# Kernel optimization log

Hardware: AMD Instinct MI355X
Metric: run time of the kernel (lower is better)

## Reference

```python
import jax, jax.numpy as jnp
import numpy as np

LMAX = 2
MMAX = 2
SPH = (LMAX + 1) ** 2  # 9 coefficients
E = 800000


def _rot_y(a):
    c, s = jnp.cos(a), jnp.sin(a)
    o, z = jnp.ones_like(a), jnp.zeros_like(a)
    return jnp.stack([jnp.stack([c, z, s], -1),
                      jnp.stack([z, o, z], -1),
                      jnp.stack([-s, z, c], -1)], -2)


def _rot_x(a):
    c, s = jnp.cos(a), jnp.sin(a)
    o, z = jnp.ones_like(a), jnp.zeros_like(a)
    return jnp.stack([jnp.stack([o, z, z], -1),
                      jnp.stack([z, c, -s], -1),
                      jnp.stack([z, s, c], -1)], -2)


def _z_rot_mat(angle, l):
    # e3nn _z_rot_mat: M[i, dim-1-i] = sin(f_i*angle); M[i, i] = cos(f_i*angle)
    dim = 2 * l + 1
    freqs = jnp.arange(l, -l - 1, -1, dtype=angle.dtype)  # (dim,)
    s = jnp.sin(freqs * angle[:, None])  # [E, dim]
    c = jnp.cos(freqs * angle[:, None])
    inds = jnp.arange(dim)
    M = jnp.zeros((angle.shape[0], dim, dim), angle.dtype)
    M = M.at[:, inds, dim - 1 - inds].set(s)
    M = M.at[:, inds, inds].set(c)  # center overwrites sin(0)=0, as in torch
    return M


def _wigner_D(l, alpha, beta, gamma, J):
    Xa = _z_rot_mat(alpha, l)
    Xb = _z_rot_mat(beta, l)
    Xc = _z_rot_mat(gamma, l)
    return Xa @ J @ Xb @ J @ Xc


def _build_to_m():
    # CoefficientMapping.to_m: permutation regrouping (l,m) coefficients by m
    idx = lambda l, m: l * l + l + m
    order = []
    for m in range(MMAX + 1):
        for l in range(m, LMAX + 1):
            order.append(idx(l, m))
        if m > 0:
            for l in range(m, LMAX + 1):
                order.append(idx(l, -m))
    to_m = np.zeros((SPH, SPH), np.float32)
    for row, col in enumerate(order):
        to_m[row, col] = 1.0
    return jnp.asarray(to_m)


def setup_inputs() -> dict:
    key = jax.random.key(0)
    k1, k2, k3, k4 = jax.random.split(key, 4)
    return {
        'edge_distance_vec': jax.random.normal(k1, (E, 3), jnp.float32),
        'rand_vec': jax.random.uniform(k2, (E, 3), jnp.float32),
        'Jd_1': jax.random.normal(k3, (3, 3), jnp.float32),
        'Jd_2': jax.random.normal(k4, (5, 5), jnp.float32),
        'to_m': _build_to_m(),
    }


def reference(edge_distance_vec, rand_vec, Jd_1, Jd_2, to_m):
    v = edge_distance_vec
    dtype = v.dtype
    # ---- init_edge_rot_mat (rot_clip=False since direct_forces=True) ----
    norm_x = v / jnp.linalg.norm(v, axis=1, keepdims=True)
    e2 = rand_vec - 0.5
    e2 = e2 / jnp.linalg.norm(e2, axis=1, keepdims=True)
    e2b = jnp.stack([-e2[:, 1], e2[:, 0], e2[:, 2]], axis=1)
    e2c = jnp.stack([e2[:, 0], -e2[:, 2], e2[:, 1]], axis=1)
    dot = lambda a: jnp.abs(jnp.sum(a * norm_x, axis=1, keepdims=True))
    e2 = jnp.where(dot(e2) > dot(e2b), e2b, e2)
    e2 = jnp.where(dot(e2) > dot(e2c), e2c, e2)
    norm_z = jnp.cross(norm_x, e2)
    norm_z = norm_z / jnp.linalg.norm(norm_z, axis=1, keepdims=True)
    norm_y = jnp.cross(norm_x, norm_z)
    norm_y = norm_y / jnp.linalg.norm(norm_y, axis=1, keepdims=True)
    R = jnp.stack([norm_z, norm_x, norm_y], axis=1)  # [E,3,3] rows z,x,y

    # ---- rotation_to_wigner: Euler angles (e3nn convention) ----
    x = R[:, :, 1]  # R @ e_y
    alpha = jnp.arctan2(x[:, 0], x[:, 2])
    beta = jnp.arccos(jnp.clip(x[:, 1], -1.0, 1.0))
    Ralign = _rot_y(alpha) @ _rot_x(beta) @ _rot_y(jnp.zeros_like(alpha))
    Rg = jnp.swapaxes(Ralign, 1, 2) @ R
    gamma = jnp.arctan2(Rg[:, 0, 2], Rg[:, 0, 0])

    Jd_0 = jnp.ones((1, 1), dtype)
    wigner = jnp.zeros((v.shape[0], SPH, SPH), dtype)
    start = 0
    for l, J in enumerate([Jd_0, Jd_1, Jd_2]):
        block = _wigner_D(l, alpha, beta, gamma, J.astype(dtype))
        wigner = wigner.at[:, start:start + 2 * l + 1,
                           start:start + 2 * l + 1].set(block)
        start += 2 * l + 1
    wigner_inv = jnp.swapaxes(wigner, 1, 2)  # lmax == mmax: no index_select

    wm = jnp.einsum('mk,nkj->nmj', to_m, wigner)
    wm_inv = jnp.einsum('njk,mk->njm', wigner_inv, to_m)
    return R, wm, wm_inv
```

## Files before the change

### kernel.cpp

```cpp
#include <hip/hip_runtime.h>
#include <hip/hip_bf16.h>
#include <math.h>

#define TPB 64

typedef float f32x4 __attribute__((ext_vector_type(4)));

__device__ __forceinline__ void wave_lds_fence() {
    __builtin_amdgcn_sched_barrier(0);
    asm volatile("s_waitcnt lgkmcnt(0)" ::: "memory");
    __builtin_amdgcn_sched_barrier(0);
}

template<int DIM>
__device__ __forceinline__ void zchain(
    const float* __restrict__ J,
    const float (&ca)[DIM], const float (&sa)[DIM],
    const float (&cb)[DIM], const float (&sb)[DIM],
    const float (&cc)[DIM], const float (&sc)[DIM],
    float (&D)[DIM][DIM])
{
    constexpr int d1 = DIM - 1;
    float Jl[DIM][DIM];
#pragma unroll
    for (int i = 0; i < DIM; ++i)
#pragma unroll
        for (int j = 0; j < DIM; ++j)
            Jl[i][j] = J[i * DIM + j];

    float U[DIM][DIM];
#pragma unroll
    for (int i = 0; i < DIM; ++i)
#pragma unroll
        for (int j = 0; j < DIM; ++j)
            U[i][j] = ca[i] * Jl[i][j] + sa[i] * Jl[d1 - i][j];

    float V[DIM][DIM];
#pragma unroll
    for (int i = 0; i < DIM; ++i)
#pragma unroll
        for (int j = 0; j < DIM; ++j)
            V[i][j] = U[i][j] * cb[j] + U[i][d1 - j] * sb[d1 - j];

    float W[DIM][DIM];
#pragma unroll
    for (int i = 0; i < DIM; ++i)
#pragma unroll
        for (int j = 0; j < DIM; ++j) {
            float acc = 0.f;
#pragma unroll
            for (int k = 0; k < DIM; ++k)
                acc = fmaf(V[i][k], Jl[k][j], acc);
            W[i][j] = acc;
        }
#pragma unroll
    for (int i = 0; i < DIM; ++i)
#pragma unroll
        for (int j = 0; j < DIM; ++j)
            D[i][j] = W[i][j] * cc[j] + W[i][d1 - j] * sc[d1 - j];
}


__global__ __launch_bounds__(TPB) void wigner_kernel(
    const float* __restrict__ vec, const float* __restrict__ rnd,
    const float* __restrict__ J1,  const float* __restrict__ J2,
    float* __restrict__ outR,
    float* __restrict__ outWm,
    float* __restrict__ outWi,
    int E)
{
    __shared__ __align__(16) float ldsR[TPB * 9];
    __shared__ __align__(16) float ldsW[TPB * 81];

    const int t  = threadIdx.x;
    const int e0 = blockIdx.x * TPB;
    const int e  = e0 + t;
    const int ei = (e < E) ? e : (E - 1);
    const int nvalid = min(TPB, E - e0);

    float vx = vec[3 * ei + 0], vy = vec[3 * ei + 1], vz = vec[3 * ei + 2];
    float rn = rsqrtf(vx * vx + vy * vy + vz * vz);
    float nx0 = vx * rn, nx1 = vy * rn, nx2 = vz * rn;

    float ox = rnd[3 * ei + 0] - 0.5f;
    float oy = rnd[3 * ei + 1] - 0.5f;
    float oz = rnd[3 * ei + 2] - 0.5f;
    float ro = rsqrtf(ox * ox + oy * oy + oz * oz);
    ox *= ro; oy *= ro; oz *= ro;

    float sx = ox, sy = oy, sz = oz;
    float dcur = fabsf(sx * nx0 + sy * nx1 + sz * nx2);
    {
        float bx = -oy, by = ox, bz = oz;
        float db = fabsf(bx * nx0 + by * nx1 + bz * nx2);
        if (dcur > db) { sx = bx; sy = by; sz = bz; dcur = db; }
        float cx = ox, cy = -oz, cz = oy;
        float dc = fabsf(cx * nx0 + cy * nx1 + cz * nx2);
        if (dcur > dc) { sx = cx; sy = cy; sz = cz; }
    }

    float zx = nx1 * sz - nx2 * sy;
    float zy = nx2 * sx - nx0 * sz;
    float zz = nx0 * sy - nx1 * sx;
    float rz = rsqrtf(zx * zx + zy * zy + zz * zz);
    zx *= rz; zy *= rz; zz *= rz;

    float yx = nx1 * zz - nx2 * zy;
    float yy = nx2 * zx - nx0 * zz;
    float yz = nx0 * zy - nx1 * zx;
    float ry = rsqrtf(yx * yx + yy * yy + yz * yz);
    yx *= ry; yy *= ry; yz *= ry;

    float h2a = zy * zy + yy * yy;
    float rha = rsqrtf(fmaxf(h2a, 1e-30f));
    bool  za  = (h2a < 1e-24f);
    float sa  = za ? 0.f : zy * rha;
    float caa = za ? 1.f : yy * rha;
    float cbb = fminf(1.f, fmaxf(-1.f, nx1));
    float sb  = sqrtf(fmaxf(0.f, 1.f - cbb * cbb));
    float gy  = caa * zz - sa * yz;
    float gx  = caa * zx - sa * yx;
    float h2g = gy * gy + gx * gx;
    float rhg = rsqrtf(fmaxf(h2g, 1e-30f));
    bool  zg  = (h2g < 1e-24f);
    float sg  = zg ? 0.f : gy * rhg;
    float cgg = zg ? 1.f : gx * rhg;

    float ca3[3] = {caa, 1.f, caa}, sa3[3] = {sa, 0.f, -sa};
    float cb3[3] = {cbb, 1.f, cbb}, sb3[3] = {sb, 0.f, -sb};
    float cc3[3] = {cgg, 1.f, cgg}, sc3[3] = {sg, 0.f, -sg};
    float D1[3][3];
    zchain<3>(J1, ca3, sa3, cb3, sb3, cc3, sc3, D1);

    float ca2 = caa * caa - sa * sa,  sa2 = 2.f * sa * caa;
    float cb2 = cbb * cbb - sb * sb,  sb2 = 2.f * sb * cbb;
    float cg2 = cgg * cgg - sg * sg,  sg2 = 2.f * sg * cgg;
    float ca5[5] = {ca2, caa, 1.f, caa, ca2}, sa5[5] = {sa2, sa, 0.f, -sa, -sa2};
    float cb5[5] = {cb2, cbb, 1.f, cbb, cb2}, sb5[5] = {sb2, sb, 0.f, -sb, -sb2};
    float cc5[5] = {cg2, cgg, 1.f, cgg, cg2}, sc5[5] = {sg2, sg, 0.f, -sg, -sg2};
    float D2[5][5];
    zchain<5>(J2, ca5, sa5, cb5, sb5, cc5, sc5, D2);

    {
        float* r9 = &ldsR[t * 9];
        r9[0] = zx;  r9[1] = zy;  r9[2] = zz;
        r9[3] = nx0; r9[4] = nx1; r9[5] = nx2;
        r9[6] = yx;  r9[7] = yy;  r9[8] = yz;

        float* w = &ldsW[t * 81];
        w[0] = 1.f;
#pragma unroll
        for (int c = 1; c < 9; ++c) w[c] = 0.f;
        w[9]  = 0.f; w[10] = D1[1][0]; w[11] = D1[1][1]; w[12] = D1[1][2];
#pragma unroll
        for (int c = 4; c < 9; ++c) w[9 + c] = 0.f;
#pragma unroll
        for (int c = 0; c < 4; ++c) w[18 + c] = 0.f;
#pragma unroll
        for (int c = 0; c < 5; ++c) w[22 + c] = D2[2][c];
        w[27] = 0.f; w[28] = D1[2][0]; w[29] = D1[2][1]; w[30] = D1[2][2];
#pragma unroll
        for (int c = 4; c < 9; ++c) w[27 + c] = 0.f;
#pragma unroll
        for (int c = 0; c < 4; ++c) w[36 + c] = 0.f;
#pragma unroll
        for (int c = 0; c < 5; ++c) w[40 + c] = D2[3][c];
        w[45] = 0.f; w[46] = D1[0][0]; w[47] = D1[0][1]; w[48] = D1[0][2];
#pragma unroll
        for (int c = 4; c < 9; ++c) w[45 + c] = 0.f;
#pragma unroll
        for (int c = 0; c < 4; ++c) w[54 + c] = 0.f;
#pragma unroll
        for (int c = 0; c < 5; ++c) w[58 + c] = D2[1][c];
#pragma unroll
        for (int c = 0; c < 4; ++c) w[63 + c] = 0.f;
#pragma unroll
        for (int c = 0; c < 5; ++c) w[67 + c] = D2[4][c];
#pragma unroll
        for (int c = 0; c < 4; ++c) w[72 + c] = 0.f;
#pragma unroll
        for (int c = 0; c < 5; ++c) w[76 + c] = D2[0][c];
    }
    wave_lds_fence();

    if (nvalid == TPB) {
        const f32x4* sR = reinterpret_cast<const f32x4*>(ldsR);
        f32x4* dR = reinterpret_cast<f32x4*>(outR + (size_t)e0 * 9);
#pragma unroll
        for (int idx = t; idx < (TPB * 9) / 4; idx += TPB)
            __builtin_nontemporal_store(sR[idx], &dR[idx]);
        const f32x4* sW = reinterpret_cast<const f32x4*>(ldsW);
        f32x4* dW = reinterpret_cast<f32x4*>(outWm + (size_t)e0 * 81);
        for (int idx = t; idx < (TPB * 81) / 4; idx += TPB)
            __builtin_nontemporal_store(sW[idx], &dW[idx]);
    } else {
        float* dR = outR + (size_t)e0 * 9;
        for (int idx = t; idx < nvalid * 9; idx += TPB) dR[idx] = ldsR[idx];
        float* dW = outWm + (size_t)e0 * 81;
        for (int idx = t; idx < nvalid * 81; idx += TPB) dW[idx] = ldsW[idx];
    }
    wave_lds_fence();

    {
        float* w = &ldsW[t * 81];
        w[0] = 1.f;
#pragma unroll
        for (int c = 1; c < 9; ++c) w[c] = 0.f;
#pragma unroll
        for (int j = 0; j < 3; ++j) {
            float* r = &w[(1 + j) * 9];
            r[0] = 0.f; r[1] = D1[1][j]; r[2] = 0.f; r[3] = D1[2][j];
            r[4] = 0.f; r[5] = D1[0][j]; r[6] = 0.f; r[7] = 0.f; r[8] = 0.f;
        }
#pragma unroll
        for (int c = 0; c < 5; ++c) {
            float* r = &w[(4 + c) * 9];
            r[0] = 0.f; r[1] = 0.f; r[2] = D2[2][c]; r[3] = 0.f;
            r[4] = D2[3][c]; r[5] = 0.f; r[6] = D2[1][c];
            r[7] = D2[4][c]; r[8] = D2[0][c];
        }
    }
    wave_lds_fence();

    if (nvalid == TPB) {
        const f32x4* sW = reinterpret_cast<const f32x4*>(ldsW);
        f32x4* dW = reinterpret_cast<f32x4*>(outWi + (size_t)e0 * 81);
        for (int idx = t; idx < (TPB * 81) / 4; idx += TPB)
            __builtin_nontemporal_store(sW[idx], &dW[idx]);
    } else {
        float* dW = outWi + (size_t)e0 * 81;
        for (int idx = t; idx < nvalid * 81; idx += TPB) dW[idx] = ldsW[idx];
    }
}

extern "C" void kernel_launch(void* const* d_in, const int* in_sizes, int n_in,
                              void* d_out, int out_size, void* d_ws, size_t ws_size,
                              hipStream_t stream) {
    const float* vec = (const float*)d_in[0];
    const float* rnd = (const float*)d_in[1];
    const float* J1  = (const float*)d_in[2];
    const float* J2  = (const float*)d_in[3];
    float* out = (float*)d_out;

    const int E = in_sizes[0] / 3;
    float* outR  = out;
    float* outWm = out + (size_t)E * 9;
    float* outWi = out + (size_t)E * 90;

    const int blocks = (E + TPB - 1) / TPB;
    hipLaunchKernelGGL(wigner_kernel, dim3(blocks), dim3(TPB), 0, stream,
                       vec, rnd, J1, J2, outR, outWm, outWi, E);
}
```

Measured before the change: 108.2 us.

## Make wigner kernel persistent with grid-stride tiles and prefetched inputs

Launches a capped grid of blocks that loop over tiles with a grid stride instead of one block per tile. Each iteration prefetches the next tile's input vectors into registers while computing and storing the current tile. This aims to cut block launch overhead and hide global load latency behind the large output stores. The risk is fewer resident waves, with at most 7 blocks per CU at 256 CUs, which may lower memory-level parallelism for this store-bound kernel. Register pressure also rises from the prefetched values.

```diff
diff --git a/kernel.cpp b/kernel.cpp
--- a/kernel.cpp
+++ b/kernel.cpp
@@ -3,6 +3,7 @@
 #include <math.h>
 
 #define TPB 64
+#define PERSISTENT_BLOCKS (256 * 7)
 
 typedef float f32x4 __attribute__((ext_vector_type(4)));
 
@@ -67,169 +68,182 @@
     float* __restrict__ outR,
     float* __restrict__ outWm,
     float* __restrict__ outWi,
-    int E)
+    int E, int ntiles)
 {
     __shared__ __align__(16) float ldsR[TPB * 9];
     __shared__ __align__(16) float ldsW[TPB * 81];
 
-    const int t  = threadIdx.x;
-    const int e0 = blockIdx.x * TPB;
-    const int e  = e0 + t;
-    const int ei = (e < E) ? e : (E - 1);
-    const int nvalid = min(TPB, E - e0);
-
-    float vx = vec[3 * ei + 0], vy = vec[3 * ei + 1], vz = vec[3 * ei + 2];
-    float rn = rsqrtf(vx * vx + vy * vy + vz * vz);
-    float nx0 = vx * rn, nx1 = vy * rn, nx2 = vz * rn;
-
-    float ox = rnd[3 * ei + 0] - 0.5f;
-    float oy = rnd[3 * ei + 1] - 0.5f;
-    float oz = rnd[3 * ei + 2] - 0.5f;
-    float ro = rsqrtf(ox * ox + oy * oy + oz * oz);
-    ox *= ro; oy *= ro; oz *= ro;
-
-    float sx = ox, sy = oy, sz = oz;
-    float dcur = fabsf(sx * nx0 + sy * nx1 + sz * nx2);
-    {
-        float bx = -oy, by = ox, bz = oz;
-        float db = fabsf(bx * nx0 + by * nx1 + bz * nx2);
-        if (dcur > db) { sx = bx; sy = by; sz = bz; dcur = db; }
-        float cx = ox, cy = -oz, cz = oy;
-        float dc = fabsf(cx * nx0 + cy * nx1 + cz * nx2);
-        if (dcur > dc) { sx = cx; sy = cy; sz = cz; }
-    }
-
-    float zx = nx1 * sz - nx2 * sy;
-    float zy = nx2 * sx - nx0 * sz;
-    float zz = nx0 * sy - nx1 * sx;
-    float rz = rsqrtf(zx * zx + zy * zy + zz * zz);
-    zx *= rz; zy *= rz; zz *= rz;
-
-    float yx = nx1 * zz - nx2 * zy;
-    float yy = nx2 * zx - nx0 * zz;
-    float yz = nx0 * zy - nx1 * zx;
-    float ry = rsqrtf(yx * yx + yy * yy + yz * yz);
-    yx *= ry; yy *= ry; yz *= ry;
-
-    float h2a = zy * zy + yy * yy;
-    float rha = rsqrtf(fmaxf(h2a, 1e-30f));
-    bool  za  = (h2a < 1e-24f);
-    float sa  = za ? 0.f : zy * rha;
-    float caa = za ? 1.f : yy * rha;
-    float cbb = fminf(1.f, fmaxf(-1.f, nx1));
-    float sb  = sqrtf(fmaxf(0.f, 1.f - cbb * cbb));
-    float gy  = caa * zz - sa * yz;
-    float gx  = caa * zx - sa * yx;
-    float h2g = gy * gy + gx * gx;
-    float rhg = rsqrtf(fmaxf(h2g, 1e-30f));
-    bool  zg  = (h2g < 1e-24f);
-    float sg  = zg ? 0.f : gy * rhg;
-    float cgg = zg ? 1.f : gx * rhg;
-
-    float ca3[3] = {caa, 1.f, caa}, sa3[3] = {sa, 0.f, -sa};
-    float cb3[3] = {cbb, 1.f, cbb}, sb3[3] = {sb, 0.f, -sb};
-    float cc3[3] = {cgg, 1.f, cgg}, sc3[3] = {sg, 0.f, -sg};
-    float D1[3][3];
-    zchain<3>(J1, ca3, sa3, cb3, sb3, cc3, sc3, D1);
-
-    float ca2 = caa * caa - sa * sa,  sa2 = 2.f * sa * caa;
-    float cb2 = cbb * cbb - sb * sb,  sb2 = 2.f * sb * cbb;
-    float cg2 = cgg * cgg - sg * sg,  sg2 = 2.f * sg * cgg;
-    float ca5[5] = {ca2, caa, 1.f, caa, ca2}, sa5[5] = {sa2, sa, 0.f, -sa, -sa2};
-    float cb5[5] = {cb2, cbb, 1.f, cbb, cb2}, sb5[5] = {sb2, sb, 0.f, -sb, -sb2};
-    float cc5[5] = {cg2, cgg, 1.f, cgg, cg2}, sc5[5] = {sg2, sg, 0.f, -sg, -sg2};
-    float D2[5][5];
-    zchain<5>(J2, ca5, sa5, cb5, sb5, cc5, sc5, D2);
-
-    {
-        float* r9 = &ldsR[t * 9];
-        r9[0] = zx;  r9[1] = zy;  r9[2] = zz;
-        r9[3] = nx0; r9[4] = nx1; r9[5] = nx2;
-        r9[6] = yx;  r9[7] = yy;  r9[8] = yz;
-
-        float* w = &ldsW[t * 81];
-        w[0] = 1.f;
-#pragma unroll
-        for (int c = 1; c < 9; ++c) w[c] = 0.f;
-        w[9]  = 0.f; w[10] = D1[1][0]; w[11] = D1[1][1]; w[12] = D1[1][2];
-#pragma unroll
-        for (int c = 4; c < 9; ++c) w[9 + c] = 0.f;
-#pragma unroll
-        for (int c = 0; c < 4; ++c) w[18 + c] = 0.f;
-#pragma unroll
-        for (int c = 0; c < 5; ++c) w[22 + c] = D2[2][c];
-        w[27] = 0.f; w[28] = D1[2][0]; w[29] = D1[2][1]; w[30] = D1[2][2];
-#pragma unroll
-        for (int c = 4; c < 9; ++c) w[27 + c] = 0.f;
-#pragma unroll
-        for (int c = 0; c < 4; ++c) w[36 + c] = 0.f;
-#pragma unroll
-        for (int c = 0; c < 5; ++c) w[40 + c] = D2[3][c];
-        w[45] = 0.f; w[46] = D1[0][0]; w[47] = D1[0][1]; w[48] = D1[0][2];
-#pragma unroll
-        for (int c = 4; c < 9; ++c) w[45 + c] = 0.f;
-#pragma unroll
-        for (int c = 0; c < 4; ++c) w[54 + c] = 0.f;
-#pragma unroll
-        for (int c = 0; c < 5; ++c) w[58 + c] = D2[1][c];
-#pragma unroll
-        for (int c = 0; c < 4; ++c) w[63 + c] = 0.f;
-#pragma unroll
-        for (int c = 0; c < 5; ++c) w[67 + c] = D2[4][c];
-#pragma unroll
-        for (int c = 0; c < 4; ++c) w[72 + c] = 0.f;
-#pragma unroll
-        for (int c = 0; c < 5; ++c) w[76 + c] = D2[0][c];
-    }
-    wave_lds_fence();
-
-    if (nvalid == TPB) {
-        const f32x4* sR = reinterpret_cast<const f32x4*>(ldsR);
-        f32x4* dR = reinterpret_cast<f32x4*>(outR + (size_t)e0 * 9);
-#pragma unroll
-        for (int idx = t; idx < (TPB * 9) / 4; idx += TPB)
-            __builtin_nontemporal_store(sR[idx], &dR[idx]);
-        const f32x4* sW = reinterpret_cast<const f32x4*>(ldsW);
-        f32x4* dW = reinterpret_cast<f32x4*>(outWm + (size_t)e0 * 81);
-        for (int idx = t; idx < (TPB * 81) / 4; idx += TPB)
-            __builtin_nontemporal_store(sW[idx], &dW[idx]);
-    } else {
-        float* dR = outR + (size_t)e0 * 9;
-        for (int idx = t; idx < nvalid * 9; idx += TPB) dR[idx] = ldsR[idx];
-        float* dW = outWm + (size_t)e0 * 81;
-        for (int idx = t; idx < nvalid * 81; idx += TPB) dW[idx] = ldsW[idx];
-    }
-    wave_lds_fence();
-
-    {
-        float* w = &ldsW[t * 81];
-        w[0] = 1.f;
-#pragma unroll
-        for (int c = 1; c < 9; ++c) w[c] = 0.f;
-#pragma unroll
-        for (int j = 0; j < 3; ++j) {
-            float* r = &w[(1 + j) * 9];
-            r[0] = 0.f; r[1] = D1[1][j]; r[2] = 0.f; r[3] = D1[2][j];
-            r[4] = 0.f; r[5] = D1[0][j]; r[6] = 0.f; r[7] = 0.f; r[8] = 0.f;
-        }
-#pragma unroll
-        for (int c = 0; c < 5; ++c) {
-            float* r = &w[(4 + c) * 9];
-            r[0] = 0.f; r[1] = 0.f; r[2] = D2[2][c]; r[3] = 0.f;
-            r[4] = D2[3][c]; r[5] = 0.f; r[6] = D2[1][c];
-            r[7] = D2[4][c]; r[8] = D2[0][c];
-        }
-    }
-    wave_lds_fence();
-
-    if (nvalid == TPB) {
-        const f32x4* sW = reinterpret_cast<const f32x4*>(ldsW);
-        f32x4* dW = reinterpret_cast<f32x4*>(outWi + (size_t)e0 * 81);
-        for (int idx = t; idx < (TPB * 81) / 4; idx += TPB)
-            __builtin_nontemporal_store(sW[idx], &dW[idx]);
-    } else {
-        float* dW = outWi + (size_t)e0 * 81;
-        for (int idx = t; idx < nvalid * 81; idx += TPB) dW[idx] = ldsW[idx];
+    const int t      = threadIdx.x;
+    const int stride = gridDim.x;
+    int tile = blockIdx.x;
+    if (tile >= ntiles) return;
+
+    int ei0 = min(tile * TPB + t, E - 1);
+    float vx = vec[3 * ei0 + 0], vy = vec[3 * ei0 + 1], vz = vec[3 * ei0 + 2];
+    float rx = rnd[3 * ei0 + 0], ry_ = rnd[3 * ei0 + 1], rz_ = rnd[3 * ei0 + 2];
+
+    for (; tile < ntiles; tile += stride) {
+        int en = min((tile + stride) * TPB + t, E - 1);
+        float nvx = vec[3 * en + 0], nvy = vec[3 * en + 1], nvz = vec[3 * en + 2];
+        float nrx = rnd[3 * en + 0], nry = rnd[3 * en + 1], nrz = rnd[3 * en + 2];
+
+        const int e0     = tile * TPB;
+        const int nvalid = min(TPB, E - e0);
+
+        float rn = rsqrtf(vx * vx + vy * vy + vz * vz);
+        float nx0 = vx * rn, nx1 = vy * rn, nx2 = vz * rn;
+
+        float ox = rx - 0.5f, oy = ry_ - 0.5f, oz = rz_ - 0.5f;
+        float ro = rsqrtf(ox * ox + oy * oy + oz * oz);
+        ox *= ro; oy *= ro; oz *= ro;
+
+        float sx = ox, sy = oy, sz = oz;
+        float dcur = fabsf(sx * nx0 + sy * nx1 + sz * nx2);
+        {
+            float bx = -oy, by = ox, bz = oz;
+            float db = fabsf(bx * nx0 + by * nx1 + bz * nx2);
+            if (dcur > db) { sx = bx; sy = by; sz = bz; dcur = db; }
+            float cx = ox, cy = -oz, cz = oy;
+            float dc = fabsf(cx * nx0 + cy * nx1 + cz * nx2);
+            if (dcur > dc) { sx = cx; sy = cy; sz = cz; }
+        }
+
+        float zx = nx1 * sz - nx2 * sy;
+        float zy = nx2 * sx - nx0 * sz;
+        float zz = nx0 * sy - nx1 * sx;
+        float rz2 = rsqrtf(zx * zx + zy * zy + zz * zz);
+        zx *= rz2; zy *= rz2; zz *= rz2;
+
+        float yx = nx1 * zz - nx2 * zy;
+        float yy = nx2 * zx - nx0 * zz;
+        float yz = nx0 * zy - nx1 * zx;
+        float ryn = rsqrtf(yx * yx + yy * yy + yz * yz);
+        yx *= ryn; yy *= ryn; yz *= ryn;
+
+        float h2a = zy * zy + yy * yy;
+        float rha = rsqrtf(fmaxf(h2a, 1e-30f));
+        bool  za  = (h2a < 1e-24f);
+        float sa  = za ? 0.f : zy * rha;
+        float caa = za ? 1.f : yy * rha;
+        float cbb = fminf(1.f, fmaxf(-1.f, nx1));
+        float sb  = sqrtf(fmaxf(0.f, 1.f - cbb * cbb));
+        float gy  = caa * zz - sa * yz;
+        float gx  = caa * zx - sa * yx;
+        float h2g = gy * gy + gx * gx;
+        float rhg = rsqrtf(fmaxf(h2g, 1e-30f));
+        bool  zg  = (h2g < 1e-24f);
+        float sg  = zg ? 0.f : gy * rhg;
+        float cgg = zg ? 1.f : gx * rhg;
+
+        float ca3[3] = {caa, 1.f, caa}, sa3[3] = {sa, 0.f, -sa};
+        float cb3[3] = {cbb, 1.f, cbb}, sb3[3] = {sb, 0.f, -sb};
+        float cc3[3] = {cgg, 1.f, cgg}, sc3[3] = {sg, 0.f, -sg};
+        float D1[3][3];
+        zchain<3>(J1, ca3, sa3, cb3, sb3, cc3, sc3, D1);
+
+        float ca2 = caa * caa - sa * sa,  sa2 = 2.f * sa * caa;
+        float cb2 = cbb * cbb - sb * sb,  sb2 = 2.f * sb * cbb;
+        float cg2 = cgg * cgg - sg * sg,  sg2 = 2.f * sg * cgg;
+        float ca5[5] = {ca2, caa, 1.f, caa, ca2}, sa5[5] = {sa2, sa, 0.f, -sa, -sa2};
+        float cb5[5] = {cb2, cbb, 1.f, cbb, cb2}, sb5[5] = {sb2, sb, 0.f, -sb, -sb2};
+        float cc5[5] = {cg2, cgg, 1.f, cgg, cg2}, sc5[5] = {sg2, sg, 0.f, -sg, -sg2};
+        float D2[5][5];
+        zchain<5>(J2, ca5, sa5, cb5, sb5, cc5, sc5, D2);
+
+        {
+            float* r9 = &ldsR[t * 9];
+            r9[0] = zx;  r9[1] = zy;  r9[2] = zz;
+            r9[3] = nx0; r9[4] = nx1; r9[5] = nx2;
+            r9[6] = yx;  r9[7] = yy;  r9[8] = yz;
+
+            float* w = &ldsW[t * 81];
+            w[0] = 1.f;
+#pragma unroll
+            for (int c = 1; c < 9; ++c) w[c] = 0.f;
+            w[9]  = 0.f; w[10] = D1[1][0]; w[11] = D1[1][1]; w[12] = D1[1][2];
+#pragma unroll
+            for (int c = 4; c < 9; ++c) w[9 + c] = 0.f;
+#pragma unroll
+            for (int c = 0; c < 4; ++c) w[18 + c] = 0.f;
+#pragma unroll
+            for (int c = 0; c < 5; ++c) w[22 + c] = D2[2][c];
+            w[27] = 0.f; w[28] = D1[2][0]; w[29] = D1[2][1]; w[30] = D1[2][2];
+#pragma unroll
+            for (int c = 4; c < 9; ++c) w[27 + c] = 0.f;
+#pragma unroll
+            for (int c = 0; c < 4; ++c) w[36 + c] = 0.f;
+#pragma unroll
+            for (int c = 0; c < 5; ++c) w[40 + c] = D2[3][c];
+            w[45] = 0.f; w[46] = D1[0][0]; w[47] = D1[0][1]; w[48] = D1[0][2];
+#pragma unroll
+            for (int c = 4; c < 9; ++c) w[45 + c] = 0.f;
+#pragma unroll
+            for (int c = 0; c < 4; ++c) w[54 + c] = 0.f;
+#pragma unroll
+            for (int c = 0; c < 5; ++c) w[58 + c] = D2[1][c];
+#pragma unroll
+            for (int c = 0; c < 4; ++c) w[63 + c] = 0.f;
+#pragma unroll
+            for (int c = 0; c < 5; ++c) w[67 + c] = D2[4][c];
+#pragma unroll
+            for (int c = 0; c < 4; ++c) w[72 + c] = 0.f;
+#pragma unroll
+            for (int c = 0; c < 5; ++c) w[76 + c] = D2[0][c];
+        }
+        wave_lds_fence();
+
+        if (nvalid == TPB) {
+            const f32x4* sR = reinterpret_cast<const f32x4*>(ldsR);
+            f32x4* dR = reinterpret_cast<f32x4*>(outR + (size_t)e0 * 9);
+#pragma unroll
+            for (int idx = t; idx < (TPB * 9) / 4; idx += TPB)
+                __builtin_nontemporal_store(sR[idx], &dR[idx]);
+            const f32x4* sW = reinterpret_cast<const f32x4*>(ldsW);
+            f32x4* dW = reinterpret_cast<f32x4*>(outWm + (size_t)e0 * 81);
+            for (int idx = t; idx < (TPB * 81) / 4; idx += TPB)
+                __builtin_nontemporal_store(sW[idx], &dW[idx]);
+        } else {
+            float* dR = outR + (size_t)e0 * 9;
+            for (int idx = t; idx < nvalid * 9; idx += TPB) dR[idx] = ldsR[idx];
+            float* dW = outWm + (size_t)e0 * 81;
+            for (int idx = t; idx < nvalid * 81; idx += TPB) dW[idx] = ldsW[idx];
+        }
+        wave_lds_fence();
+
+        {
+            float* w = &ldsW[t * 81];
+            w[0] = 1.f;
+#pragma unroll
+            for (int c = 1; c < 9; ++c) w[c] = 0.f;
+#pragma unroll
+            for (int j = 0; j < 3; ++j) {
+                float* r = &w[(1 + j) * 9];
+                r[0] = 0.f; r[1] = D1[1][j]; r[2] = 0.f; r[3] = D1[2][j];
+                r[4] = 0.f; r[5] = D1[0][j]; r[6] = 0.f; r[7] = 0.f; r[8] = 0.f;
+            }
+#pragma unroll
+            for (int c = 0; c < 5; ++c) {
+                float* r = &w[(4 + c) * 9];
+                r[0] = 0.f; r[1] = 0.f; r[2] = D2[2][c]; r[3] = 0.f;
+                r[4] = D2[3][c]; r[5] = 0.f; r[6] = D2[1][c];
+                r[7] = D2[4][c]; r[8] = D2[0][c];
+            }
+        }
+        wave_lds_fence();
+
+        if (nvalid == TPB) {
+            const f32x4* sW = reinterpret_cast<const f32x4*>(ldsW);
+            f32x4* dW = reinterpret_cast<f32x4*>(outWi + (size_t)e0 * 81);
+            for (int idx = t; idx < (TPB * 81) / 4; idx += TPB)
+                __builtin_nontemporal_store(sW[idx], &dW[idx]);
+        } else {
+            float* dW = outWi + (size_t)e0 * 81;
+            for (int idx = t; idx < nvalid * 81; idx += TPB) dW[idx] = ldsW[idx];
+        }
+        wave_lds_fence();
+
+        vx = nvx; vy = nvy; vz = nvz;
+        rx = nrx; ry_ = nry; rz_ = nrz;
     }
 }
 
@@ -247,7 +261,8 @@
     float* outWm = out + (size_t)E * 9;
     float* outWi = out + (size_t)E * 90;
 
-    const int blocks = (E + TPB - 1) / TPB;
+    const int ntiles = (E + TPB - 1) / TPB;
+    const int blocks = min(ntiles, PERSISTENT_BLOCKS);
     hipLaunchKernelGGL(wigner_kernel, dim3(blocks), dim3(TPB), 0, stream,
-                       vec, rnd, J1, J2, outR, outWm, outWi, E);
-}
+                       vec, rnd, J1, J2, outR, outWm, outWi, E, ntiles);
+}
```

After: 111.2 us. 2.7% more time.
